# Kernel tuning notes

Measured on AMD Instinct MI355X. Metric: run time of the kernel, lower is better.

## Reference

```python
import jax, jax.numpy as jnp
import numpy as np

B, L, D = 1, 2048, 4096
H, KV, HD = 32, 8, 128
ROT = 64  # head_dim * partial_rotary_factor
SCALE = HD ** -0.5
NEG = -1e9


def _apply_rope(x, cos, sin):
    # x: [B, h, L, HD]; rotate only the first ROT dims (partial rotary, rotate-half convention)
    xr, xp = x[..., :ROT], x[..., ROT:]
    x1, x2 = jnp.split(xr, 2, axis=-1)
    rotated = jnp.concatenate([-x2, x1], axis=-1)
    xr = xr * cos[None, None] + rotated * sin[None, None]
    return jnp.concatenate([xr, xp], axis=-1)


def setup_inputs() -> dict:
    key = jax.random.key(0)
    k1, k2, k3 = jax.random.split(key, 3)
    x = jax.random.normal(k1, (B, L, D), jnp.float32)
    w_qkv = jax.random.normal(k2, (D, H * HD + 2 * KV * HD), jnp.float32) * 0.02
    w_o = jax.random.normal(k3, (H * HD, D), jnp.float32) * 0.02
    # causal additive mask, broadcast over batch and heads
    causal = jnp.tril(jnp.ones((L, L), dtype=bool))
    attention_mask = jnp.where(causal, 0.0, NEG).astype(jnp.float32)[None, None]
    # rotary tables over the ROT rotary dims
    inv_freq = 1.0 / (10000.0 ** (jnp.arange(0, ROT, 2, dtype=jnp.float32) / ROT))
    t = jnp.arange(L, dtype=jnp.float32)
    freqs = jnp.outer(t, inv_freq)            # [L, ROT/2]
    emb = jnp.concatenate([freqs, freqs], -1)  # [L, ROT]
    cos, sin = jnp.cos(emb), jnp.sin(emb)
    return {"x": x, "attention_mask": attention_mask, "cos": cos, "sin": sin,
            "w_qkv": w_qkv, "w_o": w_o}


def reference(x, attention_mask, cos, sin, w_qkv, w_o):
    Bx, Lx, _ = x.shape
    qkv = x @ w_qkv                                   # [B, L, H*HD + 2*KV*HD]
    q_pos = H * HD
    kv_pos = q_pos + KV * HD
    q = qkv[:, :, :q_pos].reshape(Bx, Lx, H, HD).transpose(0, 2, 1, 3)
    k = qkv[:, :, q_pos:kv_pos].reshape(Bx, Lx, KV, HD).transpose(0, 2, 1, 3)
    v = qkv[:, :, kv_pos:].reshape(Bx, Lx, KV, HD).transpose(0, 2, 1, 3)
    q = _apply_rope(q, cos, sin)
    k = _apply_rope(k, cos, sin)
    # GQA: duplicate KV heads (as in the original module)
    n_rep = H // KV
    k = jnp.repeat(k, n_rep, axis=1)
    v = jnp.repeat(v, n_rep, axis=1)
    w = jnp.einsum("bhqd,bhkd->bhqk", q, k) * SCALE   # [B, H, L, L]
    w = jax.nn.softmax(w + attention_mask, axis=-1)
    o = jnp.einsum("bhqk,bhkd->bhqd", w, v)           # [B, H, L, HD]
    o = o.transpose(0, 2, 1, 3).reshape(Bx, Lx, H * HD)
    return o @ w_o
```

## Files before the change

kernel.cpp:

```cpp
#include <hip/hip_runtime.h>
#include <stdint.h>

typedef float f32x4 __attribute__((ext_vector_type(4)));
typedef short s16x8 __attribute__((ext_vector_type(8)));
typedef unsigned short u16x4 __attribute__((ext_vector_type(4)));
typedef unsigned short u16x8 __attribute__((ext_vector_type(8)));

#define SCALE_F 0.08838834764831845f

__device__ __forceinline__ unsigned short f32_to_bf16(float f) {
    union { float f; unsigned int u; } v; v.f = f;
    return (unsigned short)((v.u + 0x7FFFu + ((v.u >> 16) & 1u)) >> 16);
}
__device__ __forceinline__ float bf16_to_f32(unsigned short h) {
    union { unsigned int u; float f; } v; v.u = (unsigned int)h << 16;
    return v.f;
}

__device__ __forceinline__ void gload16(const void* g, void* l) {
    __builtin_amdgcn_global_load_lds((const __attribute__((address_space(1))) unsigned int*)g,
                                     (__attribute__((address_space(3))) unsigned int*)l,
                                     16, 0, 0);
}

__global__ void k_conv_bf16(const float* __restrict__ in, unsigned short* __restrict__ out, int n4) {
    int i = blockIdx.x * 256 + threadIdx.x;
    if (i >= n4) return;
    f32x4 v = ((const f32x4*)in)[i];
    u16x4 o;
    o[0] = f32_to_bf16(v[0]); o[1] = f32_to_bf16(v[1]);
    o[2] = f32_to_bf16(v[2]); o[3] = f32_to_bf16(v[3]);
    ((u16x4*)out)[i] = o;
}

__global__ void k_transpose_f32(const float* __restrict__ in, unsigned short* __restrict__ out,
                                int R, int in_ld, int in_off) {
    __shared__ float tile[64][65];
    const int rb = blockIdx.y * 64, cb = blockIdx.x * 64;
    const int t = threadIdx.x;
    const int lr = t >> 4, lc4 = (t & 15) * 4;
#pragma unroll
    for (int i = 0; i < 4; ++i) {
        int r = i * 16 + lr;
        f32x4 v = *(const f32x4*)(in + (size_t)(rb + r) * in_ld + in_off + cb + lc4);
        tile[r][lc4 + 0] = v[0]; tile[r][lc4 + 1] = v[1];
        tile[r][lc4 + 2] = v[2]; tile[r][lc4 + 3] = v[3];
    }
    __syncthreads();
#pragma unroll
    for (int i = 0; i < 4; ++i) {
        int oc = cb + i * 16 + lr;
        u16x4 o;
#pragma unroll
        for (int j = 0; j < 4; ++j)
            o[j] = f32_to_bf16(tile[lc4 + j][i * 16 + lr]);
        *(u16x4*)(out + (size_t)oc * R + rb + lc4) = o;
    }
}

__global__ void k_transpose_b16(const unsigned short* __restrict__ in, unsigned short* __restrict__ out,
                                int R, int in_ld, int in_off) {
    __shared__ unsigned short tile[64][68];
    const int rb = blockIdx.y * 64, cb = blockIdx.x * 64;
    const int t = threadIdx.x;
    const int lr = t >> 4, lc4 = (t & 15) * 4;
#pragma unroll
    for (int i = 0; i < 4; ++i) {
        int r = i * 16 + lr;
        u16x4 v = *(const u16x4*)(in + (size_t)(rb + r) * in_ld + in_off + cb + lc4);
        tile[r][lc4 + 0] = v[0]; tile[r][lc4 + 1] = v[1];
        tile[r][lc4 + 2] = v[2]; tile[r][lc4 + 3] = v[3];
    }
    __syncthreads();
#pragma unroll
    for (int i = 0; i < 4; ++i) {
        int oc = cb + i * 16 + lr;
        u16x4 o;
#pragma unroll
        for (int j = 0; j < 4; ++j)
            o[j] = tile[lc4 + j][i * 16 + lr];
        *(u16x4*)(out + (size_t)oc * R + rb + lc4) = o;
    }
}

template<int BN, typename OUT>
__global__ __launch_bounds__(512, 1)
void k_gemm8p(const unsigned short* __restrict__ A, const unsigned short* __restrict__ Bt,
              OUT* __restrict__ C, int N, int K) {
    constexpr int BH = BN * 32;
    constexpr int NF = BN / 64;
    __shared__ __align__(16) unsigned short As[2][2][8192];
    __shared__ __align__(16) unsigned short Bs[2][2][BH];
    const int tid = threadIdx.x;
    const int lane = tid & 63, wid = tid >> 6;
    const int g = lane >> 4, l15 = lane & 15;
    const int wm = wid >> 2, wn = wid & 3;
    const int nwg = gridDim.x, bid = blockIdx.x;
    const int swz = (bid & 7) * (nwg >> 3) + (bid >> 3);
    const int ntn = N / BN;
    const int bm = swz / ntn, bn = swz - bm * ntn;
    const int brow = bm << 8, bcol = bn * BN;

    const int rS = tid >> 2;
    const int kcS = (tid & 3) ^ (rS & 3) ^ ((rS >> 2) & 3);
    const unsigned short* sA = A + (size_t)(brow + rS) * K + kcS * 8;
    const unsigned short* sB = Bt + (size_t)(bcol + rS) * K + kcS * 8;
    const int fsw = (g ^ (l15 & 3) ^ ((l15 >> 2) & 3)) * 8;

    f32x4 acc[8][NF] = {};
    const int nt = K >> 6;

    auto stA = [&](int t, int kh) {
        unsigned short* d = &As[t & 1][kh][tid * 8];
        const unsigned short* s = sA + (size_t)t * 64 + kh * 32;
        gload16(s, d);
        gload16(s + (size_t)128 * K, d + 4096);
    };
    auto stB = [&](int t, int kh) {
        unsigned short* d = &Bs[t & 1][kh][tid * 8];
        const unsigned short* s = sB + (size_t)t * 64 + kh * 32;
        gload16(s, d);
        if constexpr (BN == 256) gload16(s + (size_t)128 * K, d + 4096);
    };

    stA(0, 0); stB(0, 0); stA(0, 1); stB(0, 1);

    for (int t = 0; t < nt; ++t) {
        const int c = t & 1;
        if constexpr (BN == 256) {
            s16x8 af[4], bf[4];
            if (t + 1 < nt) { stA(t + 1, 0); asm volatile("s_waitcnt vmcnt(6)" ::: "memory"); }
            else            { asm volatile("s_waitcnt vmcnt(4)" ::: "memory"); }
            __builtin_amdgcn_s_barrier();
#pragma unroll
            for (int f = 0; f < 4; ++f)
                af[f] = *(const s16x8*)(&As[c][0][(wm * 128 + f * 16 + l15) * 32 + fsw]);
#pragma unroll
            for (int j = 0; j < 4; ++j)
                bf[j] = *(const s16x8*)(&Bs[c][0][(wn * 64 + j * 16 + l15) * 32 + fsw]);
            __builtin_amdgcn_s_setprio(1);
#pragma unroll
            for (int f = 0; f < 4; ++f)
#pragma unroll
                for (int j = 0; j < 4; ++j)
                    acc[f][j] = __builtin_amdgcn_mfma_f32_16x16x32_bf16(af[f], bf[j], acc[f][j], 0, 0, 0);
            __builtin_amdgcn_s_setprio(0);
            if (t + 1 < nt) stB(t + 1, 0);
#pragma unroll
            for (int f = 0; f < 4; ++f)
                af[f] = *(const s16x8*)(&As[c][0][(wm * 128 + 64 + f * 16 + l15) * 32 + fsw]);
            __builtin_amdgcn_s_setprio(1);
#pragma unroll
            for (int f = 0; f < 4; ++f)
#pragma unroll
                for (int j = 0; j < 4; ++j)
                    acc[4 + f][j] = __builtin_amdgcn_mfma_f32_16x16x32_bf16(af[f], bf[j], acc[4 + f][j], 0, 0, 0);
            __builtin_amdgcn_s_setprio(0);
            if (t + 1 < nt) { stA(t + 1, 1); asm volatile("s_waitcnt vmcnt(4)" ::: "memory"); }
            else            { asm volatile("s_waitcnt vmcnt(0)" ::: "memory"); }
            __builtin_amdgcn_s_barrier();
#pragma unroll
            for (int f = 0; f < 4; ++f)
                af[f] = *(const s16x8*)(&As[c][1][(wm * 128 + f * 16 + l15) * 32 + fsw]);
#pragma unroll
            for (int j = 0; j < 4; ++j)
                bf[j] = *(const s16x8*)(&Bs[c][1][(wn * 64 + j * 16 + l15) * 32 + fsw]);
            __builtin_amdgcn_s_setprio(1);
#pragma unroll
            for (int f = 0; f < 4; ++f)
#pragma unroll
                for (int j = 0; j < 4; ++j)
                    acc[f][j] = __builtin_amdgcn_mfma_f32_16x16x32_bf16(af[f], bf[j], acc[f][j], 0, 0, 0);
            __builtin_amdgcn_s_setprio(0);
            if (t + 1 < nt) stB(t + 1, 1);
#pragma unroll
            for (int f = 0; f < 4; ++f)
                af[f] = *(const s16x8*)(&As[c][1][(wm * 128 + 64 + f * 16 + l15) * 32 + fsw]);
            __builtin_amdgcn_s_setprio(1);
#pragma unroll
            for (int f = 0; f < 4; ++f)
#pragma unroll
                for (int j = 0; j < 4; ++j)
                    acc[4 + f][j] = __builtin_amdgcn_mfma_f32_16x16x32_bf16(af[f], bf[j], acc[4 + f][j], 0, 0, 0);
            __builtin_amdgcn_s_setprio(0);
        } else {
            s16x8 af[8], bf[2];
            if (t + 1 < nt) { stA(t + 1, 0); stB(t + 1, 0); asm volatile("s_waitcnt vmcnt(6)" ::: "memory"); }
            else            { asm volatile("s_waitcnt vmcnt(3)" ::: "memory"); }
            __builtin_amdgcn_s_barrier();
#pragma unroll
            for (int f = 0; f < 8; ++f)
                af[f] = *(const s16x8*)(&As[c][0][(wm * 128 + f * 16 + l15) * 32 + fsw]);
#pragma unroll
            for (int j = 0; j < 2; ++j)
                bf[j] = *(const s16x8*)(&Bs[c][0][(wn * 32 + j * 16 + l15) * 32 + fsw]);
            __builtin_amdgcn_s_setprio(1);
#pragma unroll
            for (int f = 0; f < 8; ++f)
#pragma unroll
                for (int j = 0; j < 2; ++j)
                    acc[f][j] = __builtin_amdgcn_mfma_f32_16x16x32_bf16(af[f], bf[j], acc[f][j], 0, 0, 0);
            __builtin_amdgcn_s_setprio(0);
            if (t + 1 < nt) { stA(t + 1, 1); stB(t + 1, 1); asm volatile("s_waitcnt vmcnt(6)" ::: "memory"); }
            else            { asm volatile("s_waitcnt vmcnt(0)" ::: "memory"); }
            __builtin_amdgcn_s_barrier();
#pragma unroll
            for (int f = 0; f < 8; ++f)
                af[f] = *(const s16x8*)(&As[c][1][(wm * 128 + f * 16 + l15) * 32 + fsw]);
#pragma unroll
            for (int j = 0; j < 2; ++j)
                bf[j] = *(const s16x8*)(&Bs[c][1][(wn * 32 + j * 16 + l15) * 32 + fsw]);
            __builtin_amdgcn_s_setprio(1);
#pragma unroll
            for (int f = 0; f < 8; ++f)
#pragma unroll
                for (int j = 0; j < 2; ++j)
                    acc[f][j] = __builtin_amdgcn_mfma_f32_16x16x32_bf16(af[f], bf[j], acc[f][j], 0, 0, 0);
            __builtin_amdgcn_s_setprio(0);
        }
    }

#pragma unroll
    for (int f = 0; f < 8; ++f)
#pragma unroll
        for (int j = 0; j < NF; ++j)
#pragma unroll
            for (int r = 0; r < 4; ++r) {
                const size_t idx = (size_t)(brow + wm * 128 + f * 16 + g * 4 + r) * N
                                   + bcol + wn * (BN / 4) + j * 16 + l15;
                if constexpr (sizeof(OUT) == 4) C[idx] = acc[f][j][r];
                else                            C[idx] = f32_to_bf16(acc[f][j][r]);
            }
}

__global__ void k_rope_pack(const unsigned short* __restrict__ qkv, const float* __restrict__ cosT,
                            const float* __restrict__ sinT, unsigned short* __restrict__ Qb,
                            unsigned short* __restrict__ Kb) {
    const int oct = blockIdx.x * 128 + threadIdx.x;
    if (oct >= 640) return;
    const int col = oct * 8;
    const int t = blockIdx.y;
    const int d = col & 127;
    u16x8 v8 = *(const u16x8*)(qkv + (size_t)t * 6144 + col);
    u16x8 o8;
    if (d < 64) {
        u16x8 p8 = *(const u16x8*)(qkv + (size_t)t * 6144 + (col ^ 32));
        f32x4 c0 = *(const f32x4*)(cosT + t * 64 + d);
        f32x4 c1 = *(const f32x4*)(cosT + t * 64 + d + 4);
        f32x4 s0 = *(const f32x4*)(sinT + t * 64 + d);
        f32x4 s1 = *(const f32x4*)(sinT + t * 64 + d + 4);
        const float sgn = (d < 32) ? -1.f : 1.f;
#pragma unroll
        for (int j = 0; j < 8; ++j) {
            float cc = (j < 4) ? c0[j] : c1[j - 4];
            float ss = (j < 4) ? s0[j] : s1[j - 4];
            float o = bf16_to_f32(v8[j]) * cc + sgn * bf16_to_f32(p8[j]) * ss;
            o8[j] = f32_to_bf16(o);
        }
    } else {
        o8 = v8;
    }
    if (col < 4096) {
        const int h = col >> 7;
        *(u16x8*)(Qb + ((size_t)h * 2048 + t) * 128 + d) = o8;
    } else {
        const int hk = (col - 4096) >> 7;
        *(u16x8*)(Kb + ((size_t)hk * 2048 + t) * 128 + d) = o8;
    }
}

__global__ __launch_bounds__(256, 2)
void k_attn(const unsigned short* __restrict__ Qb, const unsigned short* __restrict__ Kb,
            const unsigned short* __restrict__ Vt, unsigned short* __restrict__ Ob) {
    __shared__ __align__(16) unsigned short Ks[2][8192];
    __shared__ __align__(16) unsigned short Vs[2][8192];
    __shared__ __align__(16) unsigned short Pl[2][4][1024];
    const int h = blockIdx.y, hk = h >> 2;
    const int qbA = blockIdx.x, qbB = 31 - qbA;
    const int tid = threadIdx.x, lane = tid & 63, wid = tid >> 6;
    const int g = lane >> 4, l15 = lane & 15;
    const int qrA = qbA * 64 + wid * 16, qrB = qbB * 64 + wid * 16;
    const int swz = (l15 & 7) << 4;

    s16x8 aqA[4], aqB[4];
#pragma unroll
    for (int kc = 0; kc < 4; ++kc) {
        aqA[kc] = *(const s16x8*)(Qb + ((size_t)h * 2048 + qrA + l15) * 128 + kc * 32 + g * 8);
        aqB[kc] = *(const s16x8*)(Qb + ((size_t)h * 2048 + qrB + l15) * 128 + kc * 32 + g * 8);
    }

    const unsigned short* gK = Kb + ((size_t)hk * 2048 + (tid & 63)) * 128 + (tid >> 6) * 8;
    const unsigned short* gV = Vt + ((size_t)hk * 128 + (tid & 127)) * 2048 + (tid >> 7) * 8;

    auto stage = [&](int kb) {
        unsigned short* dK = Ks[kb & 1] + tid * 8;
        unsigned short* dV = Vs[kb & 1] + tid * 8;
        const unsigned short* sK = gK + (size_t)kb * 8192;
        const unsigned short* sV = gV + kb * 64;
#pragma unroll
        for (int i = 0; i < 4; ++i) gload16(sK + i * 32, dK + i * 2048);
#pragma unroll
        for (int i = 0; i < 4; ++i) gload16(sV + i * 16, dV + i * 2048);
    };

    f32x4 oaccA[8] = {}, oaccB[8] = {};
    float mA = -1e30f, lA = 0.f, mB = -1e30f, lB = 0.f;

    auto process = [&](const s16x8* aq, f32x4* oacc, float& mr, float& lr, int qrow0,
                       char* pw, const unsigned short* ks, const unsigned short* vs, int kb) {
        f32x4 s[4] = {};
        __builtin_amdgcn_s_setprio(1);
#pragma unroll
        for (int kc = 0; kc < 4; ++kc)
#pragma unroll
            for (int kt = 0; kt < 4; ++kt) {
                s16x8 kf = *(const s16x8*)(ks + ((kc * 4 + g) * 64 + kt * 16 + l15) * 8);
                s[kt] = __builtin_amdgcn_mfma_f32_16x16x32_bf16(kf, aq[kc], s[kt], 0, 0, 0);
            }
        __builtin_amdgcn_s_setprio(0);
        const int q = qrow0 + l15;
        if (kb * 64 + 63 > qrow0) {
#pragma unroll
            for (int kt = 0; kt < 4; ++kt)
#pragma unroll
                for (int r = 0; r < 4; ++r) {
                    float xv = s[kt][r] * SCALE_F;
                    s[kt][r] = (kb * 64 + kt * 16 + g * 4 + r > q) ? -3e38f : xv;
                }
        } else {
#pragma unroll
            for (int kt = 0; kt < 4; ++kt)
#pragma unroll
                for (int r = 0; r < 4; ++r) s[kt][r] *= SCALE_F;
        }
        float mx = -3e38f;
#pragma unroll
        for (int kt = 0; kt < 4; ++kt)
#pragma unroll
            for (int r = 0; r < 4; ++r) mx = fmaxf(mx, s[kt][r]);
        mx = fmaxf(mx, __shfl_xor(mx, 16));
        mx = fmaxf(mx, __shfl_xor(mx, 32));
        if (!__all(mx - mr <= 8.0f)) {
            const float mnew = fmaxf(mr, mx);
            const float scal = __expf(mr - mnew);
            mr = mnew;
            float so[4];
#pragma unroll
            for (int r = 0; r < 4; ++r) so[r] = __shfl(scal, g * 4 + r, 16);
#pragma unroll
            for (int j = 0; j < 8; ++j) {
                oacc[j][0] *= so[0]; oacc[j][1] *= so[1];
                oacc[j][2] *= so[2]; oacc[j][3] *= so[3];
            }
            lr *= scal;
        }
        float ps = 0.f;
#pragma unroll
        for (int kt = 0; kt < 4; ++kt)
#pragma unroll
            for (int r = 0; r < 4; ++r) {
                float p = __expf(s[kt][r] - mr);
                s[kt][r] = p;
                ps += p;
            }
        ps += __shfl_xor(ps, 16);
        ps += __shfl_xor(ps, 32);
        lr += ps;
#pragma unroll
        for (int kt = 0; kt < 4; ++kt) {
            unsigned int w0 = (unsigned int)f32_to_bf16(s[kt][0]) | ((unsigned int)f32_to_bf16(s[kt][1]) << 16);
            unsigned int w1 = (unsigned int)f32_to_bf16(s[kt][2]) | ((unsigned int)f32_to_bf16(s[kt][3]) << 16);
            const int b0 = (l15 * 128 + kt * 32 + g * 8) ^ swz;
            *(unsigned int*)(pw + b0) = w0;
            *(unsigned int*)(pw + b0 + 4) = w1;
        }
        __builtin_amdgcn_s_setprio(1);
#pragma unroll
        for (int kc = 0; kc < 2; ++kc) {
            s16x8 pa = *(const s16x8*)(pw + ((l15 * 128 + kc * 64 + g * 16) ^ swz));
#pragma unroll
            for (int j = 0; j < 8; ++j) {
                s16x8 bv = *(const s16x8*)(vs + ((kc * 4 + g) * 128 + j * 16 + l15) * 8);
                oacc[j] = __builtin_amdgcn_mfma_f32_16x16x32_bf16(pa, bv, oacc[j], 0, 0, 0);
            }
        }
        __builtin_amdgcn_s_setprio(0);
    };

    const int nkb = qbB + 1;
    stage(0);
    for (int kb = 0; kb < nkb; ++kb) {
        if (kb + 1 < nkb) {
            stage(kb + 1);
            asm volatile("s_waitcnt vmcnt(8)" ::: "memory");
        } else {
            asm volatile("s_waitcnt vmcnt(0)" ::: "memory");
        }
        __builtin_amdgcn_s_barrier();
        const unsigned short* ks = Ks[kb & 1];
        const unsigned short* vs = Vs[kb & 1];
        process(aqB, oaccB, mB, lB, qrB, (char*)Pl[1][wid], ks, vs, kb);
        if (kb <= qbA)
            process(aqA, oaccA, mA, lA, qrA, (char*)Pl[0][wid], ks, vs, kb);
        __builtin_amdgcn_s_barrier();
    }
    float liA[4], liB[4];
#pragma unroll
    for (int r = 0; r < 4; ++r) {
        liA[r] = 1.f / __shfl(lA, g * 4 + r, 16);
        liB[r] = 1.f / __shfl(lB, g * 4 + r, 16);
    }
#pragma unroll
    for (int j = 0; j < 8; ++j)
#pragma unroll
        for (int r = 0; r < 4; ++r) {
            Ob[(size_t)(qrA + g * 4 + r) * 4096 + h * 128 + j * 16 + l15] = f32_to_bf16(oaccA[j][r] * liA[r]);
            Ob[(size_t)(qrB + g * 4 + r) * 4096 + h * 128 + j * 16 + l15] = f32_to_bf16(oaccB[j][r] * liB[r]);
        }
}

extern "C" void kernel_launch(void* const* d_in, const int* in_sizes, int n_in,
                              void* d_out, int out_size, void* d_ws, size_t ws_size,
                              hipStream_t stream) {
    const float* x     = (const float*)d_in[0];
    const float* cosT  = (const float*)d_in[2];
    const float* sinT  = (const float*)d_in[3];
    const float* w_qkv = (const float*)d_in[4];
    const float* w_o   = (const float*)d_in[5];
    float* out = (float*)d_out;

    char* ws = (char*)d_ws;
    unsigned short* wT   = (unsigned short*)(ws + 0);
    unsigned short* qkvb = (unsigned short*)(ws + 50331648);
    unsigned short* Ob   = (unsigned short*)(ws + 50331648);
    unsigned short* xb   = (unsigned short*)(ws + 100663296);
    unsigned short* Qb   = xb;
    unsigned short* Kb   = (unsigned short*)(ws + 117440512);
    unsigned short* Vt   = (unsigned short*)(ws + 121634816);

    k_conv_bf16<<<8192, 256, 0, stream>>>(x, xb, 2097152);
    k_transpose_f32<<<dim3(96, 64), 256, 0, stream>>>(w_qkv, wT, 4096, 6144, 0);
    k_gemm8p<256, unsigned short><<<192, 512, 0, stream>>>(xb, wT, qkvb, 6144, 4096);
    k_rope_pack<<<dim3(5, 2048), 128, 0, stream>>>(qkvb, cosT, sinT, Qb, Kb);
    k_transpose_b16<<<dim3(16, 32), 256, 0, stream>>>(qkvb, Vt, 2048, 6144, 5120);
    k_transpose_f32<<<dim3(64, 64), 256, 0, stream>>>(w_o, wT, 4096, 4096, 0);
    k_attn<<<dim3(16, 32), 256, 0, stream>>>(Qb, Kb, Vt, Ob);
    k_gemm8p<128, float><<<256, 512, 0, stream>>>(Ob, wT, out, 4096, 4096);
}
```

Baseline: 363.6 us.

## Fuse RoPE and Q/K head packing into QKV GEMM epilogue; interleave attention QK stages

A dedicated QKV GEMM kernel now applies rotary embedding and writes Q and K directly in head-major layout from its accumulators. V goes to a compact temporary buffer that is then transposed. This removes the separate rope_pack kernel and the full qkv intermediate round trip. In the attention kernel, the QK matmuls for both query blocks are issued before either softmax, which may improve MFMA/ALU overlap at the cost of more live registers. The epilogue now does scalar, less coalesced stores and per-element cos/sin loads.

```diff
diff --git a/kernel.cpp b/kernel.cpp
--- a/kernel.cpp
+++ b/kernel.cpp
@@ -4,17 +4,12 @@
 typedef float f32x4 __attribute__((ext_vector_type(4)));
 typedef short s16x8 __attribute__((ext_vector_type(8)));
 typedef unsigned short u16x4 __attribute__((ext_vector_type(4)));
-typedef unsigned short u16x8 __attribute__((ext_vector_type(8)));
 
 #define SCALE_F 0.08838834764831845f
 
 __device__ __forceinline__ unsigned short f32_to_bf16(float f) {
     union { float f; unsigned int u; } v; v.f = f;
     return (unsigned short)((v.u + 0x7FFFu + ((v.u >> 16) & 1u)) >> 16);
-}
-__device__ __forceinline__ float bf16_to_f32(unsigned short h) {
-    union { unsigned int u; float f; } v; v.u = (unsigned int)h << 16;
-    return v.f;
 }
 
 __device__ __forceinline__ void gload16(const void* g, void* l) {
@@ -80,6 +75,147 @@
         for (int j = 0; j < 4; ++j)
             o[j] = tile[lc4 + j][i * 16 + lr];
         *(u16x4*)(out + (size_t)oc * R + rb + lc4) = o;
+    }
+}
+
+__global__ __launch_bounds__(512, 1)
+void k_gemmA(const unsigned short* __restrict__ A, const unsigned short* __restrict__ Bt,
+             unsigned short* __restrict__ Qb, unsigned short* __restrict__ Kb,
+             unsigned short* __restrict__ Vtmp,
+             const float* __restrict__ cosT, const float* __restrict__ sinT,
+             int N, int K) {
+    __shared__ __align__(16) unsigned short As[2][2][8192];
+    __shared__ __align__(16) unsigned short Bs[2][2][8192];
+    const int tid = threadIdx.x;
+    const int lane = tid & 63, wid = tid >> 6;
+    const int g = lane >> 4, l15 = lane & 15;
+    const int wm = wid >> 2, wn = wid & 3;
+    const int nwg = gridDim.x, bid = blockIdx.x;
+    const int swz = (bid & 7) * (nwg >> 3) + (bid >> 3);
+    const int ntn = N >> 8;
+    const int bm = swz / ntn, bn = swz - bm * ntn;
+    const int brow = bm << 8, bcol = bn << 8;
+
+    const int rS = tid >> 2;
+    const int kcS = (tid & 3) ^ (rS & 3) ^ ((rS >> 2) & 3);
+    const unsigned short* sA = A + (size_t)(brow + rS) * K + kcS * 8;
+    const unsigned short* sB = Bt + (size_t)(bcol + rS) * K + kcS * 8;
+    const int fsw = (g ^ (l15 & 3) ^ ((l15 >> 2) & 3)) * 8;
+
+    f32x4 acc[8][4] = {};
+    const int nt = K >> 6;
+
+    auto stA = [&](int t, int kh) {
+        unsigned short* d = &As[t & 1][kh][tid * 8];
+        const unsigned short* s = sA + (size_t)t * 64 + kh * 32;
+        gload16(s, d);
+        gload16(s + (size_t)128 * K, d + 4096);
+    };
+    auto stB = [&](int t, int kh) {
+        unsigned short* d = &Bs[t & 1][kh][tid * 8];
+        const unsigned short* s = sB + (size_t)t * 64 + kh * 32;
+        gload16(s, d);
+        gload16(s + (size_t)128 * K, d + 4096);
+    };
+
+    stA(0, 0); stB(0, 0); stA(0, 1); stB(0, 1);
+
+    for (int t = 0; t < nt; ++t) {
+        const int c = t & 1;
+        s16x8 af[4], bf[4];
+        if (t + 1 < nt) { stA(t + 1, 0); asm volatile("s_waitcnt vmcnt(6)" ::: "memory"); }
+        else            { asm volatile("s_waitcnt vmcnt(4)" ::: "memory"); }
+        __builtin_amdgcn_s_barrier();
+#pragma unroll
+        for (int f = 0; f < 4; ++f)
+            af[f] = *(const s16x8*)(&As[c][0][(wm * 128 + f * 16 + l15) * 32 + fsw]);
+#pragma unroll
+        for (int j = 0; j < 4; ++j)
+            bf[j] = *(const s16x8*)(&Bs[c][0][(wn * 64 + j * 16 + l15) * 32 + fsw]);
+        __builtin_amdgcn_s_setprio(1);
+#pragma unroll
+        for (int f = 0; f < 4; ++f)
+#pragma unroll
+            for (int j = 0; j < 4; ++j)
+                acc[f][j] = __builtin_amdgcn_mfma_f32_16x16x32_bf16(af[f], bf[j], acc[f][j], 0, 0, 0);
+        __builtin_amdgcn_s_setprio(0);
+        if (t + 1 < nt) stB(t + 1, 0);
+#pragma unroll
+        for (int f = 0; f < 4; ++f)
+            af[f] = *(const s16x8*)(&As[c][0][(wm * 128 + 64 + f * 16 + l15) * 32 + fsw]);
+        __builtin_amdgcn_s_setprio(1);
+#pragma unroll
+        for (int f = 0; f < 4; ++f)
+#pragma unroll
+            for (int j = 0; j < 4; ++j)
+                acc[4 + f][j] = __builtin_amdgcn_mfma_f32_16x16x32_bf16(af[f], bf[j], acc[4 + f][j], 0, 0, 0);
+        __builtin_amdgcn_s_setprio(0);
+        if (t + 1 < nt) { stA(t + 1, 1); asm volatile("s_waitcnt vmcnt(4)" ::: "memory"); }
+        else            { asm volatile("s_waitcnt vmcnt(0)" ::: "memory"); }
+        __builtin_amdgcn_s_barrier();
+#pragma unroll
+        for (int f = 0; f < 4; ++f)
+            af[f] = *(const s16x8*)(&As[c][1][(wm * 128 + f * 16 + l15) * 32 + fsw]);
+#pragma unroll
+        for (int j = 0; j < 4; ++j)
+            bf[j] = *(const s16x8*)(&Bs[c][1][(wn * 64 + j * 16 + l15) * 32 + fsw]);
+        __builtin_amdgcn_s_setprio(1);
+#pragma unroll
+        for (int f = 0; f < 4; ++f)
+#pragma unroll
+            for (int j = 0; j < 4; ++j)
+                acc[f][j] = __builtin_amdgcn_mfma_f32_16x16x32_bf16(af[f], bf[j], acc[f][j], 0, 0, 0);
+        __builtin_amdgcn_s_setprio(0);
+        if (t + 1 < nt) stB(t + 1, 1);
+#pragma unroll
+        for (int f = 0; f < 4; ++f)
+            af[f] = *(const s16x8*)(&As[c][1][(wm * 128 + 64 + f * 16 + l15) * 32 + fsw]);
+        __builtin_amdgcn_s_setprio(1);
+#pragma unroll
+        for (int f = 0; f < 4; ++f)
+#pragma unroll
+            for (int j = 0; j < 4; ++j)
+                acc[4 + f][j] = __builtin_amdgcn_mfma_f32_16x16x32_bf16(af[f], bf[j], acc[4 + f][j], 0, 0, 0);
+        __builtin_amdgcn_s_setprio(0);
+    }
+
+    const int colb = bcol + wn * 64;
+    const bool ropehalf = ((colb & 64) == 0);
+    const bool isV = (colb >= 5120);
+    unsigned short* base0 = nullptr;
+    if (!isV) {
+        base0 = (colb < 4096)
+            ? Qb + ((size_t)(colb >> 7) * 2048) * 128 + (colb & 64)
+            : Kb + ((size_t)((colb - 4096) >> 7) * 2048) * 128 + (colb & 64);
+    }
+#pragma unroll
+    for (int f = 0; f < 8; ++f) {
+#pragma unroll
+        for (int r = 0; r < 4; ++r) {
+            const int row = brow + wm * 128 + f * 16 + g * 4 + r;
+            if (isV) {
+#pragma unroll
+                for (int j = 0; j < 4; ++j)
+                    Vtmp[(size_t)row * 1024 + (colb - 5120) + j * 16 + l15] = f32_to_bf16(acc[f][j][r]);
+            } else if (ropehalf) {
+                unsigned short* dst = base0 + (size_t)row * 128;
+#pragma unroll
+                for (int j = 0; j < 4; ++j) {
+                    const int d = j * 16 + l15;
+                    const float cc = cosT[row * 64 + d];
+                    const float ss = sinT[row * 64 + d];
+                    const float p = acc[f][j ^ 2][r];
+                    const float o = (j < 2) ? (acc[f][j][r] * cc - p * ss)
+                                            : (acc[f][j][r] * cc + p * ss);
+                    dst[d] = f32_to_bf16(o);
+                }
+            } else {
+                unsigned short* dst = base0 + (size_t)row * 128;
+#pragma unroll
+                for (int j = 0; j < 4; ++j)
+                    dst[j * 16 + l15] = f32_to_bf16(acc[f][j][r]);
+            }
+        }
     }
 }
 
@@ -127,97 +263,39 @@
 
     for (int t = 0; t < nt; ++t) {
         const int c = t & 1;
-        if constexpr (BN == 256) {
-            s16x8 af[4], bf[4];
-            if (t + 1 < nt) { stA(t + 1, 0); asm volatile("s_waitcnt vmcnt(6)" ::: "memory"); }
-            else            { asm volatile("s_waitcnt vmcnt(4)" ::: "memory"); }
-            __builtin_amdgcn_s_barrier();
-#pragma unroll
-            for (int f = 0; f < 4; ++f)
-                af[f] = *(const s16x8*)(&As[c][0][(wm * 128 + f * 16 + l15) * 32 + fsw]);
-#pragma unroll
-            for (int j = 0; j < 4; ++j)
-                bf[j] = *(const s16x8*)(&Bs[c][0][(wn * 64 + j * 16 + l15) * 32 + fsw]);
-            __builtin_amdgcn_s_setprio(1);
-#pragma unroll
-            for (int f = 0; f < 4; ++f)
-#pragma unroll
-                for (int j = 0; j < 4; ++j)
-                    acc[f][j] = __builtin_amdgcn_mfma_f32_16x16x32_bf16(af[f], bf[j], acc[f][j], 0, 0, 0);
-            __builtin_amdgcn_s_setprio(0);
-            if (t + 1 < nt) stB(t + 1, 0);
-#pragma unroll
-            for (int f = 0; f < 4; ++f)
-                af[f] = *(const s16x8*)(&As[c][0][(wm * 128 + 64 + f * 16 + l15) * 32 + fsw]);
-            __builtin_amdgcn_s_setprio(1);
-#pragma unroll
-            for (int f = 0; f < 4; ++f)
-#pragma unroll
-                for (int j = 0; j < 4; ++j)
-                    acc[4 + f][j] = __builtin_amdgcn_mfma_f32_16x16x32_bf16(af[f], bf[j], acc[4 + f][j], 0, 0, 0);
-            __builtin_amdgcn_s_setprio(0);
-            if (t + 1 < nt) { stA(t + 1, 1); asm volatile("s_waitcnt vmcnt(4)" ::: "memory"); }
-            else            { asm volatile("s_waitcnt vmcnt(0)" ::: "memory"); }
-            __builtin_amdgcn_s_barrier();
-#pragma unroll
-            for (int f = 0; f < 4; ++f)
-                af[f] = *(const s16x8*)(&As[c][1][(wm * 128 + f * 16 + l15) * 32 + fsw]);
-#pragma unroll
-            for (int j = 0; j < 4; ++j)
-                bf[j] = *(const s16x8*)(&Bs[c][1][(wn * 64 + j * 16 + l15) * 32 + fsw]);
-            __builtin_amdgcn_s_setprio(1);
-#pragma unroll
-            for (int f = 0; f < 4; ++f)
-#pragma unroll
-                for (int j = 0; j < 4; ++j)
-                    acc[f][j] = __builtin_amdgcn_mfma_f32_16x16x32_bf16(af[f], bf[j], acc[f][j], 0, 0, 0);
-            __builtin_amdgcn_s_setprio(0);
-            if (t + 1 < nt) stB(t + 1, 1);
-#pragma unroll
-            for (int f = 0; f < 4; ++f)
-                af[f] = *(const s16x8*)(&As[c][1][(wm * 128 + 64 + f * 16 + l15) * 32 + fsw]);
-            __builtin_amdgcn_s_setprio(1);
-#pragma unroll
-            for (int f = 0; f < 4; ++f)
-#pragma unroll
-                for (int j = 0; j < 4; ++j)
-                    acc[4 + f][j] = __builtin_amdgcn_mfma_f32_16x16x32_bf16(af[f], bf[j], acc[4 + f][j], 0, 0, 0);
-            __builtin_amdgcn_s_setprio(0);
-        } else {
-            s16x8 af[8], bf[2];
-            if (t + 1 < nt) { stA(t + 1, 0); stB(t + 1, 0); asm volatile("s_waitcnt vmcnt(6)" ::: "memory"); }
-            else            { asm volatile("s_waitcnt vmcnt(3)" ::: "memory"); }
-            __builtin_amdgcn_s_barrier();
-#pragma unroll
-            for (int f = 0; f < 8; ++f)
-                af[f] = *(const s16x8*)(&As[c][0][(wm * 128 + f * 16 + l15) * 32 + fsw]);
+        s16x8 af[8], bf[2];
+        if (t + 1 < nt) { stA(t + 1, 0); stB(t + 1, 0); asm volatile("s_waitcnt vmcnt(6)" ::: "memory"); }
+        else            { asm volatile("s_waitcnt vmcnt(3)" ::: "memory"); }
+        __builtin_amdgcn_s_barrier();
+#pragma unroll
+        for (int f = 0; f < 8; ++f)
+            af[f] = *(const s16x8*)(&As[c][0][(wm * 128 + f * 16 + l15) * 32 + fsw]);
+#pragma unroll
+        for (int j = 0; j < 2; ++j)
+            bf[j] = *(const s16x8*)(&Bs[c][0][(wn * 32 + j * 16 + l15) * 32 + fsw]);
+        __builtin_amdgcn_s_setprio(1);
+#pragma unroll
+        for (int f = 0; f < 8; ++f)
 #pragma unroll
             for (int j = 0; j < 2; ++j)
-                bf[j] = *(const s16x8*)(&Bs[c][0][(wn * 32 + j * 16 + l15) * 32 + fsw]);
-            __builtin_amdgcn_s_setprio(1);
-#pragma unroll
-            for (int f = 0; f < 8; ++f)
-#pragma unroll
-                for (int j = 0; j < 2; ++j)
-                    acc[f][j] = __builtin_amdgcn_mfma_f32_16x16x32_bf16(af[f], bf[j], acc[f][j], 0, 0, 0);
-            __builtin_amdgcn_s_setprio(0);
-            if (t + 1 < nt) { stA(t + 1, 1); stB(t + 1, 1); asm volatile("s_waitcnt vmcnt(6)" ::: "memory"); }
-            else            { asm volatile("s_waitcnt vmcnt(0)" ::: "memory"); }
-            __builtin_amdgcn_s_barrier();
-#pragma unroll
-            for (int f = 0; f < 8; ++f)
-                af[f] = *(const s16x8*)(&As[c][1][(wm * 128 + f * 16 + l15) * 32 + fsw]);
+                acc[f][j] = __builtin_amdgcn_mfma_f32_16x16x32_bf16(af[f], bf[j], acc[f][j], 0, 0, 0);
+        __builtin_amdgcn_s_setprio(0);
+        if (t + 1 < nt) { stA(t + 1, 1); stB(t + 1, 1); asm volatile("s_waitcnt vmcnt(6)" ::: "memory"); }
+        else            { asm volatile("s_waitcnt vmcnt(0)" ::: "memory"); }
+        __builtin_amdgcn_s_barrier();
+#pragma unroll
+        for (int f = 0; f < 8; ++f)
+            af[f] = *(const s16x8*)(&As[c][1][(wm * 128 + f * 16 + l15) * 32 + fsw]);
+#pragma unroll
+        for (int j = 0; j < 2; ++j)
+            bf[j] = *(const s16x8*)(&Bs[c][1][(wn * 32 + j * 16 + l15) * 32 + fsw]);
+        __builtin_amdgcn_s_setprio(1);
+#pragma unroll
+        for (int f = 0; f < 8; ++f)
 #pragma unroll
             for (int j = 0; j < 2; ++j)
-                bf[j] = *(const s16x8*)(&Bs[c][1][(wn * 32 + j * 16 + l15) * 32 + fsw]);
-            __builtin_amdgcn_s_setprio(1);
-#pragma unroll
-            for (int f = 0; f < 8; ++f)
-#pragma unroll
-                for (int j = 0; j < 2; ++j)
-                    acc[f][j] = __builtin_amdgcn_mfma_f32_16x16x32_bf16(af[f], bf[j], acc[f][j], 0, 0, 0);
-            __builtin_amdgcn_s_setprio(0);
-        }
+                acc[f][j] = __builtin_amdgcn_mfma_f32_16x16x32_bf16(af[f], bf[j], acc[f][j], 0, 0, 0);
+        __builtin_amdgcn_s_setprio(0);
     }
 
 #pragma unroll
@@ -231,42 +309,6 @@
                 if constexpr (sizeof(OUT) == 4) C[idx] = acc[f][j][r];
                 else                            C[idx] = f32_to_bf16(acc[f][j][r]);
             }
-}
-
-__global__ void k_rope_pack(const unsigned short* __restrict__ qkv, const float* __restrict__ cosT,
-                            const float* __restrict__ sinT, unsigned short* __restrict__ Qb,
-                            unsigned short* __restrict__ Kb) {
-    const int oct = blockIdx.x * 128 + threadIdx.x;
-    if (oct >= 640) return;
-    const int col = oct * 8;
-    const int t = blockIdx.y;
-    const int d = col & 127;
-    u16x8 v8 = *(const u16x8*)(qkv + (size_t)t * 6144 + col);
-    u16x8 o8;
-    if (d < 64) {
-        u16x8 p8 = *(const u16x8*)(qkv + (size_t)t * 6144 + (col ^ 32));
-        f32x4 c0 = *(const f32x4*)(cosT + t * 64 + d);
-        f32x4 c1 = *(const f32x4*)(cosT + t * 64 + d + 4);
-        f32x4 s0 = *(const f32x4*)(sinT + t * 64 + d);
-        f32x4 s1 = *(const f32x4*)(sinT + t * 64 + d + 4);
-        const float sgn = (d < 32) ? -1.f : 1.f;
-#pragma unroll
-        for (int j = 0; j < 8; ++j) {
-            float cc = (j < 4) ? c0[j] : c1[j - 4];
-            float ss = (j < 4) ? s0[j] : s1[j - 4];
-            float o = bf16_to_f32(v8[j]) * cc + sgn * bf16_to_f32(p8[j]) * ss;
-            o8[j] = f32_to_bf16(o);
-        }
-    } else {
-        o8 = v8;
-    }
-    if (col < 4096) {
-        const int h = col >> 7;
-        *(u16x8*)(Qb + ((size_t)h * 2048 + t) * 128 + d) = o8;
-    } else {
-        const int hk = (col - 4096) >> 7;
-        *(u16x8*)(Kb + ((size_t)hk * 2048 + t) * 128 + d) = o8;
-    }
 }
 
 __global__ __launch_bounds__(256, 2)
@@ -306,9 +348,7 @@
     f32x4 oaccA[8] = {}, oaccB[8] = {};
     float mA = -1e30f, lA = 0.f, mB = -1e30f, lB = 0.f;
 
-    auto process = [&](const s16x8* aq, f32x4* oacc, float& mr, float& lr, int qrow0,
-                       char* pw, const unsigned short* ks, const unsigned short* vs, int kb) {
-        f32x4 s[4] = {};
+    auto qk = [&](const s16x8* aq, f32x4* s, const unsigned short* ks) {
         __builtin_amdgcn_s_setprio(1);
 #pragma unroll
         for (int kc = 0; kc < 4; ++kc)
@@ -318,6 +358,9 @@
                 s[kt] = __builtin_amdgcn_mfma_f32_16x16x32_bf16(kf, aq[kc], s[kt], 0, 0, 0);
             }
         __builtin_amdgcn_s_setprio(0);
+    };
+
+    auto sm = [&](f32x4* s, f32x4* oacc, float& mr, float& lr, int qrow0, int kb, char* pw) {
         const int q = qrow0 + l15;
         if (kb * 64 + 63 > qrow0) {
 #pragma unroll
@@ -374,6 +417,9 @@
             *(unsigned int*)(pw + b0) = w0;
             *(unsigned int*)(pw + b0 + 4) = w1;
         }
+    };
+
+    auto pv = [&](f32x4* oacc, char* pw, const unsigned short* vs) {
         __builtin_amdgcn_s_setprio(1);
 #pragma unroll
         for (int kc = 0; kc < 2; ++kc) {
@@ -399,9 +445,16 @@
         __builtin_amdgcn_s_barrier();
         const unsigned short* ks = Ks[kb & 1];
         const unsigned short* vs = Vs[kb & 1];
-        process(aqB, oaccB, mB, lB, qrB, (char*)Pl[1][wid], ks, vs, kb);
-        if (kb <= qbA)
-            process(aqA, oaccA, mA, lA, qrA, (char*)Pl[0][wid], ks, vs, kb);
+        const bool doA = (kb <= qbA);
+        f32x4 sB_[4] = {}, sA_[4] = {};
+        qk(aqB, sB_, ks);
+        if (doA) qk(aqA, sA_, ks);
+        sm(sB_, oaccB, mB, lB, qrB, kb, (char*)Pl[1][wid]);
+        pv(oaccB, (char*)Pl[1][wid], vs);
+        if (doA) {
+            sm(sA_, oaccA, mA, lA, qrA, kb, (char*)Pl[0][wid]);
+            pv(oaccA, (char*)Pl[0][wid], vs);
+        }
         __builtin_amdgcn_s_barrier();
     }
     float liA[4], liB[4];
@@ -431,18 +484,17 @@
 
     char* ws = (char*)d_ws;
     unsigned short* wT   = (unsigned short*)(ws + 0);
-    unsigned short* qkvb = (unsigned short*)(ws + 50331648);
-    unsigned short* Ob   = (unsigned short*)(ws + 50331648);
-    unsigned short* xb   = (unsigned short*)(ws + 100663296);
-    unsigned short* Qb   = xb;
-    unsigned short* Kb   = (unsigned short*)(ws + 117440512);
-    unsigned short* Vt   = (unsigned short*)(ws + 121634816);
+    unsigned short* Qb   = (unsigned short*)(ws + 50331648);
+    unsigned short* Kb   = (unsigned short*)(ws + 67108864);
+    unsigned short* Vtmp = (unsigned short*)(ws + 71303168);
+    unsigned short* Vt   = (unsigned short*)(ws + 75497472);
+    unsigned short* xb   = (unsigned short*)(ws + 79691776);
+    unsigned short* Ob   = (unsigned short*)(ws + 96468992);
 
     k_conv_bf16<<<8192, 256, 0, stream>>>(x, xb, 2097152);
     k_transpose_f32<<<dim3(96, 64), 256, 0, stream>>>(w_qkv, wT, 4096, 6144, 0);
-    k_gemm8p<256, unsigned short><<<192, 512, 0, stream>>>(xb, wT, qkvb, 6144, 4096);
-    k_rope_pack<<<dim3(5, 2048), 128, 0, stream>>>(qkvb, cosT, sinT, Qb, Kb);
-    k_transpose_b16<<<dim3(16, 32), 256, 0, stream>>>(qkvb, Vt, 2048, 6144, 5120);
+    k_gemmA<<<192, 512, 0, stream>>>(xb, wT, Qb, Kb, Vtmp, cosT, sinT, 6144, 4096);
+    k_transpose_b16<<<dim3(16, 32), 256, 0, stream>>>(Vtmp, Vt, 2048, 1024, 0);
     k_transpose_f32<<<dim3(64, 64), 256, 0, stream>>>(w_o, wT, 4096, 4096, 0);
     k_attn<<<dim3(16, 32), 256, 0, stream>>>(Qb, Kb, Vt, Ob);
     k_gemm8p<128, float><<<256, 512, 0, stream>>>(Ob, wT, out, 4096, 4096);
```

New measurement: 373.3 us. +2.7%, slower.
